# Performance work log

Measured on AMD Instinct MI355X. Metric: run time of the kernel, lower is better.

The kernel has to match this reference:

```python
import jax, jax.numpy as jnp
import numpy as np

N, M, C = 32768, 8192, 128
K = 3            # number of interpolation neighbors (PointNet++/RepSurf FP)
EPS_BN = 1e-5    # torch BatchNorm1d default eps
EPS_D = 1e-8     # RepSurf dist_recip eps


def setup_inputs() -> dict:
    key = jax.random.key(0)
    ks = jax.random.split(key, 16)
    s = 0.05
    inp = {
        "pos1": jax.random.normal(ks[0], (N, 3), jnp.float32),
        "pos2": jax.random.normal(ks[1], (M, 3), jnp.float32),
        "feat2": jax.random.normal(ks[2], (M, C), jnp.float32),
    }
    # MLP stack [128,128,128]: Linear + BatchNorm1d (gamma/beta) per layer
    for i in range(3):
        inp[f"W{i}"] = jax.random.normal(ks[3 + i], (C, C), jnp.float32) * s
        inp[f"b{i}"] = jnp.zeros((C,), jnp.float32)
        inp[f"g{i}"] = jnp.ones((C,), jnp.float32)
        inp[f"be{i}"] = jnp.zeros((C,), jnp.float32)
    return inp


def _lin_bn_relu(x, W, b, g, be):
    # Linear -> BatchNorm1d (training-mode batch stats, biased var) -> ReLU
    y = x @ W.T + b
    m = y.mean(axis=0)
    v = y.var(axis=0)
    return jax.nn.relu((y - m) * jax.lax.rsqrt(v + EPS_BN) * g + be)


def reference(pos1, pos2, feat2, W0, b0, g0, be0, W1, b1, g1, be1, W2, b2, g2, be2):
    # squared pairwise distances [N, M] (memory-bound: 1 GB fp32)
    d = ((pos1 ** 2).sum(-1, keepdims=True)
         + (pos2 ** 2).sum(-1)[None, :]
         - 2.0 * (pos1 @ pos2.T))
    neg_d, idx = jax.lax.top_k(-d, K)          # 3 nearest neighbors
    dk = jnp.maximum(-neg_d, 0.0)              # [N, K] squared dists
    w = 1.0 / (dk + EPS_D)
    w = w / w.sum(-1, keepdims=True)           # inverse-distance weights
    # gather neighbor features and interpolate: [N, K, C] -> [N, C]
    interp = jnp.einsum('nkc,nk->nc', feat2[idx], w)
    x = _lin_bn_relu(interp, W0, b0, g0, be0)
    x = _lin_bn_relu(x, W1, b1, g1, be1)
    x = _lin_bn_relu(x, W2, b2, g2, be2)
    return x
```

## Files before the change

### kernel.cpp

```cpp
#include <hip/hip_runtime.h>
#include <math.h>

#define NQ 32768
#define MC 8192
#define CC 128
#define EPS_BN 1e-5f
#define EPS_D  1e-8

#define DBL_BIG 1e300
#define IDX_BIG 0x7fffffff

#define QB  64
#define TB  256
#define NW  4
#define PCE (MC / 4)
#define SLCW (PCE / NW)
#define NG  (SLCW / 4)
#define KMASK 0xFFFFE000u
#define IMASK 0x1FFFu
#define NSURV 48
#define KNN_B ((NQ / QB) * 4)
#define GEMM_B (NQ / 64)
#define NGRP 8

typedef __attribute__((ext_vector_type(8))) short bf16x8;
typedef __attribute__((ext_vector_type(4))) float floatx4;
typedef unsigned short ushort_t;

__device__ __forceinline__ unsigned bf16pair(float a, float b) {
    unsigned ua = __float_as_uint(a); ua = (ua + 0x7FFFu + ((ua >> 16) & 1u)) >> 16;
    unsigned ub = __float_as_uint(b); ub = (ub + 0x7FFFu + ((ub >> 16) & 1u)) >> 16;
    return ua | (ub << 16);
}
__device__ __forceinline__ ushort_t bf16one(float a) {
    unsigned ua = __float_as_uint(a);
    return (ushort_t)((ua + 0x7FFFu + ((ua >> 16) & 1u)) >> 16);
}
__device__ __forceinline__ float bflo(unsigned u) { return __uint_as_float(u << 16); }
__device__ __forceinline__ float bfhi(unsigned u) { return __uint_as_float(u & 0xFFFF0000u); }

__device__ __forceinline__ void ins3(float& k0, float& k1, float& k2, float x) {
    const float n0 = fminf(k0, x);
    const float n1 = __builtin_amdgcn_fmed3f(k0, k1, x);
    const float n2 = __builtin_amdgcn_fmed3f(k1, k2, x);
    k0 = n0; k1 = n1; k2 = n2;
}

__device__ __forceinline__ float mkk(float nx, float ny, float nz, float hp,
                                     float4 c, unsigned j) {
    float t = c.w + hp;
    t = fmaf(nz, c.z, t);
    t = fmaf(ny, c.y, t);
    t = fmaf(nx, c.x, t);
    const unsigned u = (__float_as_uint(t) & KMASK) | (j & ~KMASK);
    return __uint_as_float(u);
}

__global__ __launch_bounds__(TB) void pack_kernel(const float* __restrict__ pos2,
                                                  float4* __restrict__ pos2pk) {
    const int c0 = blockIdx.x * (MC / 8);
#pragma unroll
    for (int c = c0 + threadIdx.x; c < c0 + MC / 8; c += TB) {
        const float x = pos2[c * 3 + 0];
        const float y = pos2[c * 3 + 1];
        const float z = pos2[c * 3 + 2];
        float4 v;
        v.x = x; v.y = y; v.z = z;
        v.w = 0.5f * fmaf(x, x, fmaf(y, y, z * z));
        pos2pk[c] = v;
    }
    if (blockIdx.x == 0 && threadIdx.x < 4) {
        float4 zf; zf.x = 0.f; zf.y = 0.f; zf.z = 0.f; zf.w = 0.f;
        pos2pk[MC + threadIdx.x] = zf;
    }
}

__global__ __launch_bounds__(TB) void knn_kernel(const float* __restrict__ pos1,
                                                 const float4* __restrict__ pos2pk,
                                                 unsigned* __restrict__ skeys,
                                                 const float* __restrict__ W0,
                                                 const float* __restrict__ W1,
                                                 const float* __restrict__ W2,
                                                 ushort_t* __restrict__ Wbf,
                                                 float* __restrict__ stats) {
    __shared__ unsigned skl[QB][13];

    if (blockIdx.x >= KNN_B) {
        const int pb = blockIdx.x - KNN_B;
        const int f = pb * TB + threadIdx.x;
        const float* Ws[3] = {W0, W1, W2};
#pragma unroll
        for (int l = 0; l < 3; ++l) {
            const float4 v = ((const float4*)Ws[l])[f];
            unsigned* dst = (unsigned*)(Wbf + (size_t)l * CC * CC);
            dst[f * 2 + 0] = bf16pair(v.x, v.y);
            dst[f * 2 + 1] = bf16pair(v.z, v.w);
        }
        if (pb == 0)
            for (int i = threadIdx.x; i < 3 * NGRP * 256; i += TB) stats[i] = 0.f;
        return;
    }

    const int piece = blockIdx.x & 3;
    const int bq    = blockIdx.x >> 2;
    const int ln = threadIdx.x & 63;
    const int wvu = __builtin_amdgcn_readfirstlane((int)(threadIdx.x >> 6));
    const int q  = bq * QB + ln;

    const float px = pos1[q * 3 + 0];
    const float py = pos1[q * 3 + 1];
    const float pz = pos1[q * 3 + 2];
    const float nx = -px, ny = -py, nz = -pz;
    const float hp = 0.5f * fmaf(px, px, fmaf(py, py, pz * pz));

    const int jb = piece * PCE + wvu * SLCW;
    const float4* cp = pos2pk + jb;

    const float KINIT = __uint_as_float(0x7F000000u);
    float k0 = KINIT, k1 = KINIT, k2 = KINIT;

#define LOADG(v0, v1, v2, v3, g) { v0 = cp[(g)*4+0]; v1 = cp[(g)*4+1]; \
                                   v2 = cp[(g)*4+2]; v3 = cp[(g)*4+3]; }
#define CONSG(v0, v1, v2, v3, g) { const unsigned j0 = (unsigned)(jb + (g)*4); \
        ins3(k0, k1, k2, mkk(nx, ny, nz, hp, v0, j0 + 0)); \
        ins3(k0, k1, k2, mkk(nx, ny, nz, hp, v1, j0 + 1)); \
        ins3(k0, k1, k2, mkk(nx, ny, nz, hp, v2, j0 + 2)); \
        ins3(k0, k1, k2, mkk(nx, ny, nz, hp, v3, j0 + 3)); }

    float4 A0, A1, A2, A3, B0, B1, B2, B3;
    LOADG(A0, A1, A2, A3, 0);
    for (int g = 0; g < NG; g += 2) {
        LOADG(B0, B1, B2, B3, g + 1);
        CONSG(A0, A1, A2, A3, g);
        LOADG(A0, A1, A2, A3, g + 2);
        CONSG(B0, B1, B2, B3, g + 1);
    }
#undef LOADG
#undef CONSG

    skl[ln][wvu * 3 + 0] = __float_as_uint(k0);
    skl[ln][wvu * 3 + 1] = __float_as_uint(k1);
    skl[ln][wvu * 3 + 2] = __float_as_uint(k2);
    __syncthreads();

    {
        const int ql = threadIdx.x >> 2;
        const int sp = (threadIdx.x & 3) * 3;
        unsigned* dst = &skeys[(size_t)(bq * QB + ql) * NSURV + piece * 12 + sp];
        dst[0] = skl[ql][sp + 0];
        dst[1] = skl[ql][sp + 1];
        dst[2] = skl[ql][sp + 2];
    }
}

template <int MODE>
__global__ __launch_bounds__(256) void gemm_mfma(const void* __restrict__ Xsrc_,
                                                 const unsigned* __restrict__ skeys,
                                                 const float* __restrict__ pos1,
                                                 const float* __restrict__ pos2,
                                                 const float* __restrict__ statsIn,
                                                 const float* __restrict__ gIn,
                                                 const float* __restrict__ beIn,
                                                 const ushort_t* __restrict__ Wb,
                                                 const float* __restrict__ bias,
                                                 ushort_t* __restrict__ Y,
                                                 float* __restrict__ statsOut) {
    __shared__ __align__(16) short xa[64][136];
    __shared__ __align__(16) short wb[128][136];
    __shared__ float blk_s[CC], blk_q[CC];
    __shared__ float sc_l[CC], sh_l[CC];

    const int row0 = blockIdx.x * 64;

    if constexpr (MODE == 0) {
        const float* feat2 = (const float*)Xsrc_;
        __shared__ int   lidx[QB][3];
        __shared__ float lw[QB][3];
        {
            double* rrd = (double*)&xa[0][0];
            int*    rri = (int*)&wb[0][0];
            const int ql = threadIdx.x >> 2;
            const int pp = threadIdx.x & 3;
            const int qg = row0 + ql;
            const double qx = (double)pos1[qg * 3 + 0];
            const double qy = (double)pos1[qg * 3 + 1];
            const double qz = (double)pos1[qg * 3 + 2];
            double b0 = DBL_BIG, b1 = DBL_BIG, b2 = DBL_BIG;
            int    j0 = IDX_BIG, j1 = IDX_BIG, j2 = IDX_BIG;
            const uint4* kp = (const uint4*)(skeys + (size_t)qg * NSURV + pp * 12);
#pragma unroll
            for (int gi = 0; gi < 3; ++gi) {
                const uint4 kk = kp[gi];
                const unsigned ks[4] = {kk.x, kk.y, kk.z, kk.w};
#pragma unroll
                for (int u = 0; u < 4; ++u) {
                    const int id = (int)(ks[u] & IMASK);
                    const double x = (double)pos2[id * 3 + 0];
                    const double y = (double)pos2[id * 3 + 1];
                    const double z = (double)pos2[id * 3 + 2];
                    const double ax = qx - x, ay = qy - y, az = qz - z;
                    const double d = ax * ax + ay * ay + az * az;
                    const bool l2 = (d < b2) || (d == b2 && id < j2);
                    if (l2) {
                        const bool l1 = (d < b1) || (d == b1 && id < j1);
                        const bool l0 = (d < b0) || (d == b0 && id < j0);
                        b2 = l1 ? b1 : d;              j2 = l1 ? j1 : id;
                        b1 = l1 ? (l0 ? b0 : d) : b1;  j1 = l1 ? (l0 ? j0 : id) : j1;
                        b0 = l0 ? d : b0;              j0 = l0 ? id : j0;
                    }
                }
            }
            const int base = (ql * 4 + pp) * 3;
            rrd[base + 0] = b0; rri[base + 0] = j0;
            rrd[base + 1] = b1; rri[base + 1] = j1;
            rrd[base + 2] = b2; rri[base + 2] = j2;
            __syncthreads();
            if (threadIdx.x < QB) {
                const int qq = threadIdx.x;
                double c0 = DBL_BIG, c1 = DBL_BIG, c2 = DBL_BIG;
                int    i0 = IDX_BIG, i1 = IDX_BIG, i2 = IDX_BIG;
#pragma unroll
                for (int s = 0; s < 12; ++s) {
                    const double d = rrd[qq * 12 + s];
                    const int   id = rri[qq * 12 + s];
                    const bool l2 = (d < c2) || (d == c2 && id < i2);
                    if (l2) {
                        const bool l1 = (d < c1) || (d == c1 && id < i1);
                        const bool l0 = (d < c0) || (d == c0 && id < i0);
                        c2 = l1 ? c1 : d;              i2 = l1 ? i1 : id;
                        c1 = l1 ? (l0 ? c0 : d) : c1;  i1 = l1 ? (l0 ? i0 : id) : i1;
                        c0 = l0 ? d : c0;              i0 = l0 ? id : i0;
                    }
                }
                const double r0 = 1.0 / (c0 + EPS_D);
                const double r1 = 1.0 / (c1 + EPS_D);
                const double r2 = 1.0 / (c2 + EPS_D);
                const double inv = 1.0 / (r0 + r1 + r2);
                lidx[qq][0] = i0; lidx[qq][1] = i1; lidx[qq][2] = i2;
                lw[qq][0] = (float)(r0 * inv);
                lw[qq][1] = (float)(r1 * inv);
                lw[qq][2] = (float)(r2 * inv);
            }
            __syncthreads();
        }
        if (threadIdx.x < CC) { blk_s[threadIdx.x] = 0.f; blk_q[threadIdx.x] = 0.f; }
#pragma unroll
        for (int e = threadIdx.x; e < 64 * 32; e += 256) {
            const int r = e >> 5, c4 = e & 31;
            const int i0 = lidx[r][0], i1 = lidx[r][1], i2 = lidx[r][2];
            const float w0 = lw[r][0], w1 = lw[r][1], w2 = lw[r][2];
            const float4 f0 = *(const float4*)&feat2[(size_t)i0 * CC + c4 * 4];
            const float4 f1 = *(const float4*)&feat2[(size_t)i1 * CC + c4 * 4];
            const float4 f2 = *(const float4*)&feat2[(size_t)i2 * CC + c4 * 4];
            float4 v;
            v.x = w0 * f0.x + w1 * f1.x + w2 * f2.x;
            v.y = w0 * f0.y + w1 * f1.y + w2 * f2.y;
            v.z = w0 * f0.z + w1 * f1.z + w2 * f2.z;
            v.w = w0 * f0.w + w1 * f1.w + w2 * f2.w;
            unsigned* dst = (unsigned*)&xa[r][0];
            dst[c4 * 2 + 0] = bf16pair(v.x, v.y);
            dst[c4 * 2 + 1] = bf16pair(v.z, v.w);
        }
    } else {
        const ushort_t* Xbf = (const ushort_t*)Xsrc_;
        if (threadIdx.x < CC) {
            const int c = threadIdx.x;
            float s = 0.f, q = 0.f;
#pragma unroll
            for (int gr = 0; gr < NGRP; ++gr) {
                s += statsIn[gr * 256 + c];
                q += statsIn[gr * 256 + CC + c];
            }
            const float m = s * (1.f / (float)NQ);
            const float v = fmaf(-m, m, q * (1.f / (float)NQ));
            const float rstd = rsqrtf(v + EPS_BN);
            const float scl = gIn[c] * rstd;
            sc_l[c] = scl;
            sh_l[c] = fmaf(-m, scl, beIn[c]);
            blk_s[c] = 0.f; blk_q[c] = 0.f;
        }
        __syncthreads();
#pragma unroll
        for (int e = threadIdx.x; e < 64 * 16; e += 256) {
            const int r = e >> 4, c8 = e & 15;
            const uint4 u = *(const uint4*)&Xbf[(size_t)(row0 + r) * CC + c8 * 8];
            const float4 s0 = *(const float4*)&sc_l[c8 * 8];
            const float4 s1 = *(const float4*)&sc_l[c8 * 8 + 4];
            const float4 h0 = *(const float4*)&sh_l[c8 * 8];
            const float4 h1 = *(const float4*)&sh_l[c8 * 8 + 4];
            const float v0 = fmaxf(fmaf(bflo(u.x), s0.x, h0.x), 0.f);
            const float v1 = fmaxf(fmaf(bfhi(u.x), s0.y, h0.y), 0.f);
            const float v2 = fmaxf(fmaf(bflo(u.y), s0.z, h0.z), 0.f);
            const float v3 = fmaxf(fmaf(bfhi(u.y), s0.w, h0.w), 0.f);
            const float v4 = fmaxf(fmaf(bflo(u.z), s1.x, h1.x), 0.f);
            const float v5 = fmaxf(fmaf(bfhi(u.z), s1.y, h1.y), 0.f);
            const float v6 = fmaxf(fmaf(bflo(u.w), s1.z, h1.z), 0.f);
            const float v7 = fmaxf(fmaf(bfhi(u.w), s1.w, h1.w), 0.f);
            uint4 o;
            o.x = bf16pair(v0, v1); o.y = bf16pair(v2, v3);
            o.z = bf16pair(v4, v5); o.w = bf16pair(v6, v7);
            *(uint4*)&xa[r][c8 * 8] = o;
        }
    }
#pragma unroll
    for (int e = threadIdx.x; e < 128 * 16; e += 256) {
        const int co = e >> 4, seg = e & 15;
        *(float4*)&wb[co][seg * 8] = *(const float4*)&Wb[(size_t)co * CC + seg * 8];
    }
    __syncthreads();

    const int lane = threadIdx.x & 63;
    const int wv = threadIdx.x >> 6;
    const int nn = lane & 15;
    const int quad = lane >> 4;

    floatx4 acc[8] = {};

    const short* arow = &xa[wv * 16 + nn][0];
#pragma unroll
    for (int ks = 0; ks < 4; ++ks) {
        const bf16x8 a = *(const bf16x8*)(arow + ks * 32 + quad * 8);
#pragma unroll
        for (int ct = 0; ct < 8; ++ct) {
            const bf16x8 b = *(const bf16x8*)(&wb[ct * 16 + nn][0] + ks * 32 + quad * 8);
            acc[ct] = __builtin_amdgcn_mfma_f32_16x16x32_bf16(a, b, acc[ct], 0, 0, 0);
        }
    }

#pragma unroll
    for (int ct = 0; ct < 8; ++ct) {
        const float bv = bias[ct * 16 + nn];
        float s = 0.f, qv = 0.f;
#pragma unroll
        for (int r = 0; r < 4; ++r) {
            acc[ct][r] += bv;
            s += acc[ct][r];
            qv = fmaf(acc[ct][r], acc[ct][r], qv);
        }
#pragma unroll
        for (int r = 0; r < 4; ++r)
            Y[(size_t)(row0 + wv * 16 + quad * 4 + r) * CC + ct * 16 + nn] = bf16one(acc[ct][r]);
        s += __shfl_xor(s, 16, 64); s += __shfl_xor(s, 32, 64);
        qv += __shfl_xor(qv, 16, 64); qv += __shfl_xor(qv, 32, 64);
        if (quad == 0) {
            atomicAdd(&blk_s[ct * 16 + nn], s);
            atomicAdd(&blk_q[ct * 16 + nn], qv);
        }
    }
    __syncthreads();
    {
        const int ch = threadIdx.x;
        const float v = (ch < CC) ? blk_s[ch] : blk_q[ch - CC];
        atomicAdd(&statsOut[(blockIdx.x & (NGRP - 1)) * 256 + ch], v);
    }
}

__global__ __launch_bounds__(256) void bn_final(const ushort_t* __restrict__ Y,
                                                const float* __restrict__ statsIn,
                                                const float* __restrict__ g,
                                                const float* __restrict__ be,
                                                float* __restrict__ out) {
    __shared__ float sc_l[CC], sh_l[CC];
    if (threadIdx.x < CC) {
        const int c = threadIdx.x;
        float s = 0.f, q = 0.f;
#pragma unroll
        for (int gr = 0; gr < NGRP; ++gr) {
            s += statsIn[gr * 256 + c];
            q += statsIn[gr * 256 + CC + c];
        }
        const float m = s * (1.f / (float)NQ);
        const float v = fmaf(-m, m, q * (1.f / (float)NQ));
        const float rstd = rsqrtf(v + EPS_BN);
        const float scl = g[c] * rstd;
        sc_l[c] = scl;
        sh_l[c] = fmaf(-m, scl, be[c]);
    }
    __syncthreads();
    const int base = blockIdx.x * 1024 + threadIdx.x;
#pragma unroll
    for (int it = 0; it < 4; ++it) {
        const int i8 = base + it * 256;
        const int c8 = (i8 & 15) * 8;
        const uint4 u = *(const uint4*)&Y[(size_t)i8 * 8];
        const float4 s0 = *(const float4*)&sc_l[c8];
        const float4 s1 = *(const float4*)&sc_l[c8 + 4];
        const float4 h0 = *(const float4*)&sh_l[c8];
        const float4 h1 = *(const float4*)&sh_l[c8 + 4];
        float4 o0, o1;
        o0.x = fmaxf(fmaf(bflo(u.x), s0.x, h0.x), 0.f);
        o0.y = fmaxf(fmaf(bfhi(u.x), s0.y, h0.y), 0.f);
        o0.z = fmaxf(fmaf(bflo(u.y), s0.z, h0.z), 0.f);
        o0.w = fmaxf(fmaf(bfhi(u.y), s0.w, h0.w), 0.f);
        o1.x = fmaxf(fmaf(bflo(u.z), s1.x, h1.x), 0.f);
        o1.y = fmaxf(fmaf(bfhi(u.z), s1.y, h1.y), 0.f);
        o1.z = fmaxf(fmaf(bflo(u.w), s1.z, h1.z), 0.f);
        o1.w = fmaxf(fmaf(bfhi(u.w), s1.w, h1.w), 0.f);
        ((float4*)out)[i8 * 2 + 0] = o0;
        ((float4*)out)[i8 * 2 + 1] = o1;
    }
}

extern "C" void kernel_launch(void* const* d_in, const int* in_sizes, int n_in,
                              void* d_out, int out_size, void* d_ws, size_t ws_size,
                              hipStream_t stream) {
    (void)in_sizes; (void)n_in; (void)out_size; (void)ws_size;

    const float* pos1  = (const float*)d_in[0];
    const float* pos2  = (const float*)d_in[1];
    const float* feat2 = (const float*)d_in[2];
    const float* Wl[3]  = {(const float*)d_in[3], (const float*)d_in[7],  (const float*)d_in[11]};
    const float* bl[3]  = {(const float*)d_in[4], (const float*)d_in[8],  (const float*)d_in[12]};
    const float* gl[3]  = {(const float*)d_in[5], (const float*)d_in[9],  (const float*)d_in[13]};
    const float* bel[3] = {(const float*)d_in[6], (const float*)d_in[10], (const float*)d_in[14]};

    float* ws = (float*)d_ws;
    ushort_t* B0 = (ushort_t*)ws;
    ushort_t* B1 = B0 + (size_t)NQ * CC;
    unsigned* skeys = (unsigned*)(B1 + (size_t)NQ * CC);
    float* stats = (float*)(skeys + (size_t)NQ * NSURV);
    ushort_t* Wbf = (ushort_t*)(stats + 3 * NGRP * 256);
    float4* pos2pk = (float4*)(Wbf + 3 * CC * CC);

    float* st0 = stats + 0 * NGRP * 256;
    float* st1 = stats + 1 * NGRP * 256;
    float* st2 = stats + 2 * NGRP * 256;

    pack_kernel<<<8, TB, 0, stream>>>(pos2, pos2pk);
    knn_kernel<<<KNN_B + 16, TB, 0, stream>>>(pos1, pos2pk, skeys,
                                              Wl[0], Wl[1], Wl[2], Wbf, stats);
    gemm_mfma<0><<<GEMM_B, 256, 0, stream>>>(feat2, skeys, pos1, pos2,
                                             nullptr, nullptr, nullptr,
                                             Wbf + 0 * CC * CC, bl[0], B0, st0);
    gemm_mfma<1><<<GEMM_B, 256, 0, stream>>>(B0, nullptr, nullptr, nullptr,
                                             st0, gl[0], bel[0],
                                             Wbf + 1 * CC * CC, bl[1], B1, st1);
    gemm_mfma<1><<<GEMM_B, 256, 0, stream>>>(B1, nullptr, nullptr, nullptr,
                                             st1, gl[1], bel[1],
                                             Wbf + 2 * CC * CC, bl[2], B0, st2);
    bn_final<<<GEMM_B, 256, 0, stream>>>(B0, st2, gl[2], bel[2], (float*)d_out);
}
```

Before: 203.3 us.

## Deepen KNN load pipeline, split GEMM columns across blocks, halve BN tile

The KNN scan now keeps four groups of candidate loads in flight instead of two, and the zero-padding tail of the packed pos2 buffer grows to cover the larger prefetch overrun. The two MODE-1 GEMM layers split the 128 output columns across two blocks, doubling the grid, and each block loads only its half of the weights and emits per-column stats atomics. bn_final uses twice as many blocks, each handling half the elements. The aim is more parallelism and memory-latency hiding, at the cost of extra register pressure in the KNN kernel and redundant A-tile loading and BN-scale setup per column split.

```diff
diff --git a/kernel.cpp b/kernel.cpp
--- a/kernel.cpp
+++ b/kernel.cpp
@@ -69,7 +69,7 @@
         v.w = 0.5f * fmaf(x, x, fmaf(y, y, z * z));
         pos2pk[c] = v;
     }
-    if (blockIdx.x == 0 && threadIdx.x < 4) {
+    if (blockIdx.x == 0 && threadIdx.x < 16) {
         float4 zf; zf.x = 0.f; zf.y = 0.f; zf.z = 0.f; zf.w = 0.f;
         pos2pk[MC + threadIdx.x] = zf;
     }
@@ -127,13 +127,19 @@
         ins3(k0, k1, k2, mkk(nx, ny, nz, hp, v2, j0 + 2)); \
         ins3(k0, k1, k2, mkk(nx, ny, nz, hp, v3, j0 + 3)); }
 
-    float4 A0, A1, A2, A3, B0, B1, B2, B3;
+    float4 A0, A1, A2, A3, B0, B1, B2, B3, C0, C1, C2, C3, D0, D1, D2, D3;
     LOADG(A0, A1, A2, A3, 0);
-    for (int g = 0; g < NG; g += 2) {
-        LOADG(B0, B1, B2, B3, g + 1);
+    LOADG(B0, B1, B2, B3, 1);
+    LOADG(C0, C1, C2, C3, 2);
+    for (int g = 0; g < NG; g += 4) {
+        LOADG(D0, D1, D2, D3, g + 3);
         CONSG(A0, A1, A2, A3, g);
-        LOADG(A0, A1, A2, A3, g + 2);
+        LOADG(A0, A1, A2, A3, g + 4);
         CONSG(B0, B1, B2, B3, g + 1);
+        LOADG(B0, B1, B2, B3, g + 5);
+        CONSG(C0, C1, C2, C3, g + 2);
+        LOADG(C0, C1, C2, C3, g + 6);
+        CONSG(D0, D1, D2, D3, g + 3);
     }
 #undef LOADG
 #undef CONSG
@@ -153,7 +159,7 @@
     }
 }
 
-template <int MODE>
+template <int MODE, int CSPLIT>
 __global__ __launch_bounds__(256) void gemm_mfma(const void* __restrict__ Xsrc_,
                                                  const unsigned* __restrict__ skeys,
                                                  const float* __restrict__ pos1,
@@ -165,12 +171,16 @@
                                                  const float* __restrict__ bias,
                                                  ushort_t* __restrict__ Y,
                                                  float* __restrict__ statsOut) {
+    constexpr int NCT = 8 / CSPLIT;
     __shared__ __align__(16) short xa[64][136];
-    __shared__ __align__(16) short wb[128][136];
-    __shared__ float blk_s[CC], blk_q[CC];
+    __shared__ __align__(16) short wb[NCT * 16][136];
+    __shared__ float blk_s[NCT * 16], blk_q[NCT * 16];
     __shared__ float sc_l[CC], sh_l[CC];
 
-    const int row0 = blockIdx.x * 64;
+    const int cb = blockIdx.x % CSPLIT;
+    const int rb = blockIdx.x / CSPLIT;
+    const int row0 = rb * 64;
+    const int colbase = cb * NCT * 16;
 
     if constexpr (MODE == 0) {
         const float* feat2 = (const float*)Xsrc_;
@@ -243,7 +253,7 @@
             }
             __syncthreads();
         }
-        if (threadIdx.x < CC) { blk_s[threadIdx.x] = 0.f; blk_q[threadIdx.x] = 0.f; }
+        if (threadIdx.x < NCT * 16) { blk_s[threadIdx.x] = 0.f; blk_q[threadIdx.x] = 0.f; }
 #pragma unroll
         for (int e = threadIdx.x; e < 64 * 32; e += 256) {
             const int r = e >> 5, c4 = e & 31;
@@ -277,7 +287,7 @@
             const float scl = gIn[c] * rstd;
             sc_l[c] = scl;
             sh_l[c] = fmaf(-m, scl, beIn[c]);
-            blk_s[c] = 0.f; blk_q[c] = 0.f;
+            if (threadIdx.x < NCT * 16) { blk_s[threadIdx.x] = 0.f; blk_q[threadIdx.x] = 0.f; }
         }
         __syncthreads();
 #pragma unroll
@@ -303,9 +313,9 @@
         }
     }
 #pragma unroll
-    for (int e = threadIdx.x; e < 128 * 16; e += 256) {
+    for (int e = threadIdx.x; e < NCT * 16 * 16; e += 256) {
         const int co = e >> 4, seg = e & 15;
-        *(float4*)&wb[co][seg * 8] = *(const float4*)&Wb[(size_t)co * CC + seg * 8];
+        *(float4*)&wb[co][seg * 8] = *(const float4*)&Wb[(size_t)(colbase + co) * CC + seg * 8];
     }
     __syncthreads();
 
@@ -314,22 +324,22 @@
     const int nn = lane & 15;
     const int quad = lane >> 4;
 
-    floatx4 acc[8] = {};
+    floatx4 acc[NCT] = {};
 
     const short* arow = &xa[wv * 16 + nn][0];
 #pragma unroll
     for (int ks = 0; ks < 4; ++ks) {
         const bf16x8 a = *(const bf16x8*)(arow + ks * 32 + quad * 8);
 #pragma unroll
-        for (int ct = 0; ct < 8; ++ct) {
+        for (int ct = 0; ct < NCT; ++ct) {
             const bf16x8 b = *(const bf16x8*)(&wb[ct * 16 + nn][0] + ks * 32 + quad * 8);
             acc[ct] = __builtin_amdgcn_mfma_f32_16x16x32_bf16(a, b, acc[ct], 0, 0, 0);
         }
     }
 
 #pragma unroll
-    for (int ct = 0; ct < 8; ++ct) {
-        const float bv = bias[ct * 16 + nn];
+    for (int ct = 0; ct < NCT; ++ct) {
+        const float bv = bias[colbase + ct * 16 + nn];
         float s = 0.f, qv = 0.f;
 #pragma unroll
         for (int r = 0; r < 4; ++r) {
@@ -339,7 +349,7 @@
         }
 #pragma unroll
         for (int r = 0; r < 4; ++r)
-            Y[(size_t)(row0 + wv * 16 + quad * 4 + r) * CC + ct * 16 + nn] = bf16one(acc[ct][r]);
+            Y[(size_t)(row0 + wv * 16 + quad * 4 + r) * CC + colbase + ct * 16 + nn] = bf16one(acc[ct][r]);
         s += __shfl_xor(s, 16, 64); s += __shfl_xor(s, 32, 64);
         qv += __shfl_xor(qv, 16, 64); qv += __shfl_xor(qv, 32, 64);
         if (quad == 0) {
@@ -349,9 +359,12 @@
     }
     __syncthreads();
     {
+        const int gr = rb & (NGRP - 1);
         const int ch = threadIdx.x;
-        const float v = (ch < CC) ? blk_s[ch] : blk_q[ch - CC];
-        atomicAdd(&statsOut[(blockIdx.x & (NGRP - 1)) * 256 + ch], v);
+        if (ch < NCT * 16)
+            atomicAdd(&statsOut[gr * 256 + colbase + ch], blk_s[ch]);
+        else if (ch < 2 * NCT * 16)
+            atomicAdd(&statsOut[gr * 256 + CC + colbase + (ch - NCT * 16)], blk_q[ch - NCT * 16]);
     }
 }
 
@@ -377,9 +390,9 @@
         sh_l[c] = fmaf(-m, scl, be[c]);
     }
     __syncthreads();
-    const int base = blockIdx.x * 1024 + threadIdx.x;
-#pragma unroll
-    for (int it = 0; it < 4; ++it) {
+    const int base = blockIdx.x * 512 + threadIdx.x;
+#pragma unroll
+    for (int it = 0; it < 2; ++it) {
         const int i8 = base + it * 256;
         const int c8 = (i8 & 15) * 8;
         const uint4 u = *(const uint4*)&Y[(size_t)i8 * 8];
@@ -429,14 +442,14 @@
     pack_kernel<<<8, TB, 0, stream>>>(pos2, pos2pk);
     knn_kernel<<<KNN_B + 16, TB, 0, stream>>>(pos1, pos2pk, skeys,
                                               Wl[0], Wl[1], Wl[2], Wbf, stats);
-    gemm_mfma<0><<<GEMM_B, 256, 0, stream>>>(feat2, skeys, pos1, pos2,
-                                             nullptr, nullptr, nullptr,
-                                             Wbf + 0 * CC * CC, bl[0], B0, st0);
-    gemm_mfma<1><<<GEMM_B, 256, 0, stream>>>(B0, nullptr, nullptr, nullptr,
-                                             st0, gl[0], bel[0],
-                                             Wbf + 1 * CC * CC, bl[1], B1, st1);
-    gemm_mfma<1><<<GEMM_B, 256, 0, stream>>>(B1, nullptr, nullptr, nullptr,
-                                             st1, gl[1], bel[1],
-                                             Wbf + 2 * CC * CC, bl[2], B0, st2);
-    bn_final<<<GEMM_B, 256, 0, stream>>>(B0, st2, gl[2], bel[2], (float*)d_out);
-}
+    gemm_mfma<0, 1><<<GEMM_B, 256, 0, stream>>>(feat2, skeys, pos1, pos2,
+                                                nullptr, nullptr, nullptr,
+                                                Wbf + 0 * CC * CC, bl[0], B0, st0);
+    gemm_mfma<1, 2><<<GEMM_B * 2, 256, 0, stream>>>(B0, nullptr, nullptr, nullptr,
+                                                    st0, gl[0], bel[0],
+                                                    Wbf + 1 * CC * CC, bl[1], B1, st1);
+    gemm_mfma<1, 2><<<GEMM_B * 2, 256, 0, stream>>>(B1, nullptr, nullptr, nullptr,
+                                                    st1, gl[1], bel[1],
+                                                    Wbf + 2 * CC * CC, bl[2], B0, st2);
+    bn_final<<<GEMM_B * 2, 256, 0, stream>>>(B0, st2, gl[2], bel[2], (float*)d_out);
+}
```

Measured after the change: 212.0 us. 1.04x slower.
